# Kernel optimization log

Hardware: AMD Instinct MI355X
Metric: run time of the kernel (lower is better)

## Reference

```python
import jax, jax.numpy as jnp
import numpy as np

B, T, D_IN, UNITS, D_OUT = 64, 2048, 64, 128, 1
ODE_UNFOLDS = 6  # fused semi-implicit Euler sub-steps per timestep


def setup_inputs() -> dict:
    key = jax.random.key(0)
    ks = jax.random.split(key, 8)
    s = lambda fan: 1.0 / np.sqrt(fan).astype(np.float32)
    return {
        "x": jax.random.normal(ks[0], (B, T, D_IN), jnp.float32),
        "kernel": jax.random.normal(ks[1], (D_IN, UNITS), jnp.float32) * s(D_IN),
        "recurrent_kernel": jax.random.normal(ks[2], (UNITS, UNITS), jnp.float32) * s(UNITS),
        "bias": jnp.zeros((UNITS,), jnp.float32),
        "tau": jax.random.uniform(ks[3], (UNITS,), jnp.float32, 0.5, 2.0),  # positive time constants
        "A": jax.random.normal(ks[4], (UNITS,), jnp.float32),  # reversal potentials
        "out_kernel": jax.random.normal(ks[5], (UNITS, D_OUT), jnp.float32) * s(UNITS),
        "out_bias": jnp.zeros((D_OUT,), jnp.float32),
    }


def _ltc_scan(x_proj, recurrent_kernel, tau, A):
    # x_proj: [B, T, U] precomputed input projection (+bias)
    dt = jnp.float32(1.0 / ODE_UNFOLDS)
    inv_tau = 1.0 / tau  # [U]

    def step(h, xp):  # h: [B,U], xp: [B,U]
        # LTC fused ODE solver: semi-implicit Euler, ODE_UNFOLDS sub-steps
        for _ in range(ODE_UNFOLDS):
            f = jax.nn.sigmoid(xp + h @ recurrent_kernel)  # gating nonlinearity
            h = (h + dt * f * A) / (1.0 + dt * (inv_tau + f))
        return h, h

    h0 = jnp.zeros((x_proj.shape[0], tau.shape[0]), x_proj.dtype)
    _, hs = jax.lax.scan(step, h0, jnp.swapaxes(x_proj, 0, 1))  # scan over time
    return jnp.swapaxes(hs, 0, 1)  # [B, T, U]


def reference(x, kernel, recurrent_kernel, bias, tau, A, out_kernel, out_bias):
    # input projection hoisted out of the recurrence (invariant across unfolds)
    x_proj = jnp.einsum("bti,iu->btu", x, kernel) + bias  # [B,T,U]
    hs = _ltc_scan(x_proj, recurrent_kernel, tau, A)       # return_sequences=True
    return hs @ out_kernel + out_bias                       # Dense(output_dim) -> [B,T,1]
```

## Files before the change

### kernel.cpp

```cpp
#include <hip/hip_runtime.h>

#define TSTEPS  2048
#define DIN     64
#define UNITS   128
#define UNFOLDS 6
#define NT      128


typedef _Float16 h16x2 __attribute__((ext_vector_type(2)));

template <int CTRL>
__device__ __forceinline__ float dpp_f(float v) {
    return __int_as_float(
        __builtin_amdgcn_mov_dpp(__float_as_int(v), CTRL, 0xF, 0xF, true));
}

__device__ __forceinline__ unsigned pack_rne(float a, float b) {
    unsigned short ua = __builtin_bit_cast(unsigned short, (_Float16)a);
    unsigned short ub = __builtin_bit_cast(unsigned short, (_Float16)b);
    return (unsigned)ua | ((unsigned)ub << 16);
}

__device__ __forceinline__ float dot2(h16x2 a, h16x2 b, float c) {
#if __has_builtin(__builtin_amdgcn_fdot2)
    return __builtin_amdgcn_fdot2(a, b, c, false);
#else
    return fmaf((float)a.x, (float)b.x, fmaf((float)a.y, (float)b.y, c));
#endif
}

__global__ __launch_bounds__(NT) void ltc_kernel(
    const float* __restrict__ x,
    const float* __restrict__ kern,
    const float* __restrict__ rk,
    const float* __restrict__ bias,
    const float* __restrict__ tau,
    const float* __restrict__ Avec,
    const float* __restrict__ okern,
    const float* __restrict__ obias,
    float* __restrict__ out)
{
    const int b    = blockIdx.x;
    const int tid  = threadIdx.x;
    const int p    = tid & 3;
    const int G    = tid >> 2;
    const int wv   = tid >> 6;
    const int lane = tid & 63;

    __shared__ __align__(16) unsigned hbuf[2][UNITS / 2];
    __shared__ float part[2];

    h16x2 w2_[16][4];
    #pragma unroll
    for (int m = 0; m < 16; ++m) {
        const float* r0 = rk + (size_t)(32 * p + 2 * m) * UNITS + 4 * G;
        const float* r1 = r0 + UNITS;
        #pragma unroll
        for (int j = 0; j < 4; ++j) {
            h16x2 v; v.x = (_Float16)r0[j]; v.y = (_Float16)r1[j];
            w2_[m][j] = v;
        }
    }
    float kk_[16][4];
    #pragma unroll
    for (int m = 0; m < 16; ++m) {
        const float* r0 = kern + (size_t)(16 * p + m) * UNITS + 4 * G;
        #pragma unroll
        for (int j = 0; j < 4; ++j) kk_[m][j] = r0[j];
    }

    const int   u_own = 4 * G + p;
    const float dt    = 1.0f / 6.0f;
    const float dtA_o  = dt * Avec[u_own];
    const float cden_o = 1.0f + dt / tau[u_own];
    const float cdp_o  = cden_o + dt;
    const float ok_o   = okern[u_own];
    float bias4[4];
    #pragma unroll
    for (int j = 0; j < 4; ++j) bias4[j] = (p == 0) ? bias[4 * G + j] : 0.0f;
    const float ob = obias[0];

    float h_own = 0.0f;
    if (tid < UNITS / 2) { hbuf[0][tid] = 0u; hbuf[1][tid] = 0u; }

    const float* xb = x + (size_t)b * TSTEPS * DIN;
    float4 xr[4];
    #pragma unroll
    for (int m = 0; m < 4; ++m) xr[m] = *(const float4*)(xb + 16 * p + 4 * m);
    __syncthreads();

    for (int t = 0; t < TSTEPS; ++t) {
        float xp[4] = {bias4[0], bias4[1], bias4[2], bias4[3]};
        {
            float xq[16];
            #pragma unroll
            for (int m = 0; m < 4; ++m) {
                xq[4 * m + 0] = xr[m].x; xq[4 * m + 1] = xr[m].y;
                xq[4 * m + 2] = xr[m].z; xq[4 * m + 3] = xr[m].w;
            }
            #pragma unroll
            for (int m = 0; m < 16; ++m)
                #pragma unroll
                for (int j = 0; j < 4; ++j)
                    xp[j] = fmaf(xq[m], kk_[m][j], xp[j]);
        }

        int tn = (t + 1 < TSTEPS) ? t + 1 : t;
        float4 xn[4];
        #pragma unroll
        for (int m = 0; m < 4; ++m)
            xn[m] = *(const float4*)(xb + (size_t)tn * DIN + 16 * p + 4 * m);

        #pragma unroll
        for (int s = 0; s < UNFOLDS; ++s) {
            h16x2 hh[16];
            {
                const uint4* hv = (const uint4*)&hbuf[s & 1][16 * p];
                *(uint4*)&hh[0]  = hv[0];
                *(uint4*)&hh[4]  = hv[1];
                *(uint4*)&hh[8]  = hv[2];
                *(uint4*)&hh[12] = hv[3];
            }

            float acc[4] = {xp[0], xp[1], xp[2], xp[3]};
            float accB[4] = {0.f, 0.f, 0.f, 0.f};
            #pragma unroll
            for (int m = 0; m < 8; ++m)
                #pragma unroll
                for (int j = 0; j < 4; ++j)
                    acc[j] = dot2(hh[m], w2_[m][j], acc[j]);
            #pragma unroll
            for (int m = 8; m < 16; ++m)
                #pragma unroll
                for (int j = 0; j < 4; ++j)
                    accB[j] = dot2(hh[m], w2_[m][j], accB[j]);
            #pragma unroll
            for (int j = 0; j < 4; ++j) acc[j] += accB[j];

            const bool b0 = (p & 1) != 0;
            const bool b1 = (p & 2) != 0;
            float k0 = b0 ? acc[1] : acc[0];
            float s0 = b0 ? acc[0] : acc[1];
            float k1 = b0 ? acc[3] : acc[2];
            float s1 = b0 ? acc[2] : acc[3];
            float r0 = k0 + dpp_f<0xB1>(s0);
            float r1 = k1 + dpp_f<0xB1>(s1);
            float k2 = b1 ? r1 : r0;
            float s2 = b1 ? r0 : r1;
            float sv = k2 + dpp_f<0x4E>(s2);

            float e   = __expf(-sv);
            float num = fmaf(h_own, e, h_own + dtA_o);
            float den = fmaf(cden_o, e, cdp_o);
            h_own = num * __builtin_amdgcn_rcpf(den);

            float hN = dpp_f<0xB1>(h_own);
            if ((p & 1) == 0)
                hbuf[(s & 1) ^ 1][2 * G + (p >> 1)] = pack_rne(h_own, hN);

            if (s == UNFOLDS - 1) {
                float q = h_own * ok_o;
                q += __shfl_xor(q, 1);
                q += __shfl_xor(q, 2);
                q += __shfl_xor(q, 4);
                q += __shfl_xor(q, 8);
                q += __shfl_xor(q, 16);
                q += __shfl_xor(q, 32);
                if (lane == 0) part[wv] = q;
            }

            asm volatile("s_waitcnt lgkmcnt(0)" ::: "memory");
            __builtin_amdgcn_sched_barrier(0);
            __builtin_amdgcn_s_barrier();
            __builtin_amdgcn_sched_barrier(0);
        }

        if (tid == 0)
            out[(size_t)b * TSTEPS + t] = part[0] + part[1] + ob;

        #pragma unroll
        for (int m = 0; m < 4; ++m) xr[m] = xn[m];
    }
}

extern "C" void kernel_launch(void* const* d_in, const int* in_sizes, int n_in,
                              void* d_out, int out_size, void* d_ws, size_t ws_size,
                              hipStream_t stream) {
    const float* x     = (const float*)d_in[0];
    const float* kern  = (const float*)d_in[1];
    const float* rk    = (const float*)d_in[2];
    const float* bias  = (const float*)d_in[3];
    const float* tau   = (const float*)d_in[4];
    const float* Avec  = (const float*)d_in[5];
    const float* okern = (const float*)d_in[6];
    const float* obias = (const float*)d_in[7];
    float* out = (float*)d_out;

    ltc_kernel<<<64, NT, 0, stream>>>(
        x, kern, rk, bias, tau, Avec, okern, obias, out);
}
```

Baseline: 4.169 ms.

## Collapse LTC recurrence to a single wavefront per batch to drop barriers

Each batch row is now handled by one 64-lane wavefront instead of two, so every thread owns two hidden units and holds twice as many recurrent and input weights in registers. This removes the per-substep s_barrier and the cross-wave partial-sum exchange, and the h buffer becomes single-buffered in LDS because wave lockstep orders the reads before the writes. The cost is double the dot2 and FMA work per thread, a longer serial dependency chain per substep, and much higher register pressure, which may cause spills.

After: 6.171 ms. 1.48x slower.

```diff
diff --git a/kernel.cpp b/kernel.cpp
--- a/kernel.cpp
+++ b/kernel.cpp
@@ -4,7 +4,6 @@
 #define DIN     64
 #define UNITS   128
 #define UNFOLDS 6
-#define NT      128
 
 
 typedef _Float16 h16x2 __attribute__((ext_vector_type(2)));
@@ -29,7 +28,7 @@
 #endif
 }
 
-__global__ __launch_bounds__(NT) void ltc_kernel(
+__global__ __launch_bounds__(64) void ltc_kernel(
     const float* __restrict__ x,
     const float* __restrict__ kern,
     const float* __restrict__ rk,
@@ -41,56 +40,59 @@
     float* __restrict__ out)
 {
     const int b    = blockIdx.x;
-    const int tid  = threadIdx.x;
-    const int p    = tid & 3;
-    const int G    = tid >> 2;
-    const int wv   = tid >> 6;
-    const int lane = tid & 63;
+    const int lane = threadIdx.x;
+    const int p    = lane & 3;
+    const int G    = lane >> 2;
 
-    __shared__ __align__(16) unsigned hbuf[2][UNITS / 2];
-    __shared__ float part[2];
+    __shared__ __align__(16) unsigned hbuf[UNITS / 2];
 
-    h16x2 w2_[16][4];
+    h16x2 w2_[16][8];
     #pragma unroll
     for (int m = 0; m < 16; ++m) {
-        const float* r0 = rk + (size_t)(32 * p + 2 * m) * UNITS + 4 * G;
+        const float* r0 = rk + (size_t)(32 * p + 2 * m) * UNITS + 8 * G;
         const float* r1 = r0 + UNITS;
         #pragma unroll
-        for (int j = 0; j < 4; ++j) {
+        for (int j = 0; j < 8; ++j) {
             h16x2 v; v.x = (_Float16)r0[j]; v.y = (_Float16)r1[j];
             w2_[m][j] = v;
         }
     }
-    float kk_[16][4];
+    float kk_[16][8];
     #pragma unroll
     for (int m = 0; m < 16; ++m) {
-        const float* r0 = kern + (size_t)(16 * p + m) * UNITS + 4 * G;
+        const float* r0 = kern + (size_t)(16 * p + m) * UNITS + 8 * G;
         #pragma unroll
-        for (int j = 0; j < 4; ++j) kk_[m][j] = r0[j];
+        for (int j = 0; j < 8; ++j) kk_[m][j] = r0[j];
     }
 
-    const int   u_own = 4 * G + p;
-    const float dt    = 1.0f / 6.0f;
-    const float dtA_o  = dt * Avec[u_own];
-    const float cden_o = 1.0f + dt / tau[u_own];
-    const float cdp_o  = cden_o + dt;
-    const float ok_o   = okern[u_own];
-    float bias4[4];
+    float bias8[8];
     #pragma unroll
-    for (int j = 0; j < 4; ++j) bias4[j] = (p == 0) ? bias[4 * G + j] : 0.0f;
-    const float ob = obias[0];
+    for (int j = 0; j < 8; ++j) bias8[j] = (p == 0) ? bias[8 * G + j] : 0.0f;
 
-    float h_own = 0.0f;
-    if (tid < UNITS / 2) { hbuf[0][tid] = 0u; hbuf[1][tid] = 0u; }
+    const int   u0 = 8 * G + 4 * (p & 1) + 2 * ((p >> 1) & 1);
+    const float dt = 1.0f / 6.0f;
+    float2 Af = *(const float2*)(Avec + u0);
+    float2 Tf = *(const float2*)(tau + u0);
+    float2 Of = *(const float2*)(okern + u0);
+    const float dtA0 = dt * Af.x, dtA1 = dt * Af.y;
+    const float cd0  = 1.0f + dt / Tf.x, cd1 = 1.0f + dt / Tf.y;
+    const float cp0  = cd0 + dt, cp1 = cd1 + dt;
+    const float ok0  = Of.x, ok1 = Of.y;
+    const float ob   = obias[0];
+    const int   waddr = 4 * G + 2 * (p & 1) + ((p >> 1) & 1);
 
-    const float* xb = x + (size_t)b * TSTEPS * DIN;
+    float h0 = 0.0f, h1 = 0.0f;
+    hbuf[lane] = 0u;
+
+    const float* xb = x + (size_t)b * TSTEPS * DIN + 16 * p;
     float4 xr[4];
     #pragma unroll
-    for (int m = 0; m < 4; ++m) xr[m] = *(const float4*)(xb + 16 * p + 4 * m);
-    __syncthreads();
+    for (int m = 0; m < 4; ++m) xr[m] = *(const float4*)(xb + 4 * m);
 
     for (int t = 0; t < TSTEPS; ++t) {
-        float xp[4] = {bias4[0], bias4[1], bias4[2], bias4[3]};
+        float xp[8];
+        #pragma unroll
+        for (int j = 0; j < 8; ++j) xp[j] = bias8[j];
         {
             float xq[16];
             #pragma unroll
@@ -101,7 +103,7 @@
             #pragma unroll
             for (int m = 0; m < 16; ++m)
                 #pragma unroll
-                for (int j = 0; j < 4; ++j)
+                for (int j = 0; j < 8; ++j)
                     xp[j] = fmaf(xq[m], kk_[m][j], xp[j]);
         }
 
@@ -109,74 +111,67 @@
         float4 xn[4];
         #pragma unroll
         for (int m = 0; m < 4; ++m)
-            xn[m] = *(const float4*)(xb + (size_t)tn * DIN + 16 * p + 4 * m);
+            xn[m] = *(const float4*)(xb + (size_t)tn * DIN + 4 * m);
 
         #pragma unroll
         for (int s = 0; s < UNFOLDS; ++s) {
             h16x2 hh[16];
             {
-                const uint4* hv = (const uint4*)&hbuf[s & 1][16 * p];
+                const uint4* hv = (const uint4*)&hbuf[16 * p];
                 *(uint4*)&hh[0]  = hv[0];
                 *(uint4*)&hh[4]  = hv[1];
                 *(uint4*)&hh[8]  = hv[2];
                 *(uint4*)&hh[12] = hv[3];
             }
 
-            float acc[4] = {xp[0], xp[1], xp[2], xp[3]};
-            float accB[4] = {0.f, 0.f, 0.f, 0.f};
+            float acc[8];
             #pragma unroll
-            for (int m = 0; m < 8; ++m)
+            for (int j = 0; j < 8; ++j) acc[j] = xp[j];
+            #pragma unroll
+            for (int m = 0; m < 16; ++m)
                 #pragma unroll
-                for (int j = 0; j < 4; ++j)
+                for (int j = 0; j < 8; ++j)
                     acc[j] = dot2(hh[m], w2_[m][j], acc[j]);
-            #pragma unroll
-            for (int m = 8; m < 16; ++m)
-                #pragma unroll
-                for (int j = 0; j < 4; ++j)
-                    accB[j] = dot2(hh[m], w2_[m][j], accB[j]);
-            #pragma unroll
-            for (int j = 0; j < 4; ++j) acc[j] += accB[j];
 
             const bool b0 = (p & 1) != 0;
             const bool b1 = (p & 2) != 0;
-            float k0 = b0 ? acc[1] : acc[0];
-            float s0 = b0 ? acc[0] : acc[1];
-            float k1 = b0 ? acc[3] : acc[2];
-            float s1 = b0 ? acc[2] : acc[3];
-            float r0 = k0 + dpp_f<0xB1>(s0);
-            float r1 = k1 + dpp_f<0xB1>(s1);
-            float k2 = b1 ? r1 : r0;
-            float s2 = b1 ? r0 : r1;
-            float sv = k2 + dpp_f<0x4E>(s2);
+            float r_[4];
+            #pragma unroll
+            for (int j = 0; j < 4; ++j) {
+                float keep = b0 ? acc[j + 4] : acc[j];
+                float send = b0 ? acc[j] : acc[j + 4];
+                r_[j] = keep + dpp_f<0xB1>(send);
+            }
+            float s0v, s1v;
+            {
+                float k0 = b1 ? r_[2] : r_[0];
+                float e0 = b1 ? r_[0] : r_[2];
+                s0v = k0 + dpp_f<0x4E>(e0);
+                float k1 = b1 ? r_[3] : r_[1];
+                float e1 = b1 ? r_[1] : r_[3];
+                s1v = k1 + dpp_f<0x4E>(e1);
+            }
 
-            float e   = __expf(-sv);
-            float num = fmaf(h_own, e, h_own + dtA_o);
-            float den = fmaf(cden_o, e, cdp_o);
-            h_own = num * __builtin_amdgcn_rcpf(den);
+            float e0 = __expf(-s0v);
+            h0 = fmaf(h0, e0, h0 + dtA0) *
+                 __builtin_amdgcn_rcpf(fmaf(cd0, e0, cp0));
+            float e1 = __expf(-s1v);
+            h1 = fmaf(h1, e1, h1 + dtA1) *
+                 __builtin_amdgcn_rcpf(fmaf(cd1, e1, cp1));
 
-            float hN = dpp_f<0xB1>(h_own);
-            if ((p & 1) == 0)
-                hbuf[(s & 1) ^ 1][2 * G + (p >> 1)] = pack_rne(h_own, hN);
+            hbuf[waddr] = pack_rne(h0, h1);
 
             if (s == UNFOLDS - 1) {
-                float q = h_own * ok_o;
+                float q = fmaf(h0, ok0, h1 * ok1);
                 q += __shfl_xor(q, 1);
                 q += __shfl_xor(q, 2);
                 q += __shfl_xor(q, 4);
                 q += __shfl_xor(q, 8);
                 q += __shfl_xor(q, 16);
                 q += __shfl_xor(q, 32);
-                if (lane == 0) part[wv] = q;
+                if (lane == 0) out[(size_t)b * TSTEPS + t] = q + ob;
             }
-
-            asm volatile("s_waitcnt lgkmcnt(0)" ::: "memory");
-            __builtin_amdgcn_sched_barrier(0);
-            __builtin_amdgcn_s_barrier();
-            __builtin_amdgcn_sched_barrier(0);
         }
-
-        if (tid == 0)
-            out[(size_t)b * TSTEPS + t] = part[0] + part[1] + ob;
 
         #pragma unroll
         for (int m = 0; m < 4; ++m) xr[m] = xn[m];
@@ -196,6 +191,6 @@
     const float* obias = (const float*)d_in[7];
     float* out = (float*)d_out;
 
-    ltc_kernel<<<64, NT, 0, stream>>>(
+    ltc_kernel<<<64, 64, 0, stream>>>(
         x, kern, rk, bias, tau, Avec, okern, obias, out);
 }
```
